# Kernel optimization log

Measured on AMD Instinct MI355X. Metric: run time of the kernel, lower is better.

## Reference

```python
import jax, jax.numpy as jnp
import numpy as np

N = 50000   # nodes
E = 800000  # edges
R = 8       # relations
B = 4       # bases
NEG = 0.2   # leaky relu slope


def setup_inputs() -> dict:
    key = jax.random.key(0)
    ks = jax.random.split(key, 20)
    s = 0.1
    rn = lambda k, sh: jax.random.normal(k, sh, dtype=jnp.float32) * s
    return {
        "x": jax.random.normal(ks[0], (N, 64), dtype=jnp.float32),
        "edge_index": jax.random.randint(ks[1], (2, E), 0, N),
        "edge_type": jax.random.randint(ks[2], (E,), 0, R),
        # RGCN layer 1 (64 -> 64), basis decomposition
        "basis1": rn(ks[3], (B, 64, 64)), "comp1": rn(ks[4], (R, B)),
        "root1": rn(ks[5], (64, 64)), "brg1": jnp.zeros((64,), jnp.float32),
        # GAT layer 1 (64 -> 32, heads=4, concat -> 128)
        "wg1": rn(ks[6], (64, 128)), "asrc1": rn(ks[7], (4, 32)),
        "adst1": rn(ks[8], (4, 32)), "bg1": jnp.zeros((128,), jnp.float32),
        # RGCN layer 2 (128 -> 32)
        "basis2": rn(ks[9], (B, 128, 32)), "comp2": rn(ks[10], (R, B)),
        "root2": rn(ks[11], (128, 32)), "brg2": jnp.zeros((32,), jnp.float32),
        # GAT layer 2 (32 -> 16, heads=4, concat=False -> mean)
        "wg2": rn(ks[12], (32, 64)), "asrc2": rn(ks[13], (4, 16)),
        "adst2": rn(ks[14], (4, 16)), "bg2": jnp.zeros((16,), jnp.float32),
    }


def rgcn(x, src, dst, etype, basis, comp, root, bias):
    """PyG RGCNConv with basis decomposition, aggr='mean' per relation."""
    n, f = x.shape
    weight = jnp.einsum('rb,bio->rio', comp, basis)          # [R, in, out]
    seg = dst * R + etype                                    # per (node, relation) segment
    msg = x[src]                                             # [E, in] gather
    sums = jax.ops.segment_sum(msg, seg, num_segments=n * R).reshape(n, R, f)
    cnt = jax.ops.segment_sum(jnp.ones((src.shape[0],), x.dtype), seg,
                              num_segments=n * R).reshape(n, R, 1)
    mean = sums / jnp.maximum(cnt, 1.0)                      # [N, R, in]
    return jnp.einsum('nri,rio->no', mean, weight) + x @ root + bias


def gat(x, src, dst, w, a_src, a_dst, bias, heads, out_ch, concat):
    """PyG GATConv: add self loops, edge softmax over incoming edges."""
    n = x.shape[0]
    loop = jnp.arange(n)
    s2 = jnp.concatenate([src, loop])
    d2 = jnp.concatenate([dst, loop])
    h = (x @ w).reshape(n, heads, out_ch)                    # [N, H, C]
    al_src = (h * a_src).sum(-1)                             # [N, H]
    al_dst = (h * a_dst).sum(-1)                             # [N, H]
    e = jax.nn.leaky_relu(al_src[s2] + al_dst[d2], NEG)      # [E2, H]
    m = jax.ops.segment_max(e, d2, num_segments=n)           # stable softmax per dst
    e = jnp.exp(e - m[d2])
    z = jax.ops.segment_sum(e, d2, num_segments=n)
    alpha = e / z[d2]                                        # [E2, H]
    msg = h[s2] * alpha[:, :, None]                          # [E2, H, C]
    out = jax.ops.segment_sum(msg, d2, num_segments=n)       # [N, H, C]
    out = out.reshape(n, heads * out_ch) if concat else out.mean(axis=1)
    return out + bias


def reference(x, edge_index, edge_type,
              basis1, comp1, root1, brg1, wg1, asrc1, adst1, bg1,
              basis2, comp2, root2, brg2, wg2, asrc2, adst2, bg2):
    src, dst = edge_index[0], edge_index[1]
    # i=0: RGCN + relu (dropout p=0)
    x = jax.nn.relu(rgcn(x, src, dst, edge_type, basis1, comp1, root1, brg1))
    # i=1 == 2*pairs-1: GAT concat, NO activation
    x = gat(x, src, dst, wg1, asrc1, adst1, bg1, heads=4, out_ch=32, concat=True)
    # i=2: RGCN + relu
    x = jax.nn.relu(rgcn(x, src, dst, edge_type, basis2, comp2, root2, brg2))
    # i=3: GAT mean-heads + relu
    x = jax.nn.relu(gat(x, src, dst, wg2, asrc2, adst2, bg2, heads=4, out_ch=16, concat=False))
    return jnp.tanh(x)
```

## Files before the change

kernel.cpp:

```cpp
#include <hip/hip_runtime.h>
#include <math.h>

#define NN 50000
#define EE 800000
#define RR 8
#define SLOPE 0.2f
#define SEGS (NN * RR)
#define NBLK ((SEGS + 255) / 256)
#define NTW ((NN + 63) / 64)

typedef __attribute__((ext_vector_type(8))) short bf16x8;
typedef __attribute__((ext_vector_type(4))) float f32x4;
typedef _Float16 f16;
typedef __attribute__((ext_vector_type(4))) _Float16 h4;
typedef __attribute__((ext_vector_type(8))) _Float16 h8;

__device__ __forceinline__ float leaky(float v) { return v >= 0.f ? v : SLOPE * v; }

__device__ __forceinline__ void fmacc(float4& a, const float4& v, float p) {
    a.x = fmaf(v.x, p, a.x);
    a.y = fmaf(v.y, p, a.y);
    a.z = fmaf(v.z, p, a.z);
    a.w = fmaf(v.w, p, a.w);
}

__device__ __forceinline__ void red4(float4& a, int m) {
    a.x += __shfl_xor(a.x, m);
    a.y += __shfl_xor(a.y, m);
    a.z += __shfl_xor(a.z, m);
    a.w += __shfl_xor(a.w, m);
}

__device__ __forceinline__ float4 h4tof4(h4 t) {
    return make_float4((float)t.x, (float)t.y, (float)t.z, (float)t.w);
}

__device__ __forceinline__ void split8(const float4& v0, const float4& v1,
                                       bf16x8& hi, bf16x8& lo) {
    float e[8] = {v0.x, v0.y, v0.z, v0.w, v1.x, v1.y, v1.z, v1.w};
    union { bf16x8 v; unsigned u[4]; } H, L;
#pragma unroll
    for (int j = 0; j < 4; j++) {
        unsigned b0 = __float_as_uint(e[2 * j]), b1 = __float_as_uint(e[2 * j + 1]);
        unsigned h0 = b0 & 0xFFFF0000u, h1 = b1 & 0xFFFF0000u;
        H.u[j] = (h0 >> 16) | h1;
        float l0 = e[2 * j] - __uint_as_float(h0);
        float l1 = e[2 * j + 1] - __uint_as_float(h1);
        L.u[j] = (__float_as_uint(l0) >> 16) | (__float_as_uint(l1) & 0xFFFF0000u);
    }
    hi = H.v;
    lo = L.v;
}

__global__ void k_count2(const int* __restrict__ dst, const int* __restrict__ et,
                         int* __restrict__ cnt2) {
    int e = blockIdx.x * 256 + threadIdx.x;
    if (e < EE) atomicAdd(&cnt2[dst[e] * RR + et[e]], 1);
}

__global__ void k_scanA(const int* __restrict__ cnt2, int* __restrict__ rp,
                        int* __restrict__ bsum) {
    __shared__ int sh[256];
    int t = threadIdx.x;
    int i = blockIdx.x * 256 + t;
    int v = (i < SEGS) ? cnt2[i] : 0;
    sh[t] = v;
    __syncthreads();
    for (int off = 1; off < 256; off <<= 1) {
        int u = (t >= off) ? sh[t - off] : 0;
        __syncthreads();
        sh[t] += u;
        __syncthreads();
    }
    if (i < SEGS) rp[i] = sh[t] - v;
    if (t == 255) bsum[blockIdx.x] = sh[255];
}

__global__ void k_scanB(int* __restrict__ bsum) {
    __shared__ int sh[256];
    int t = threadIdx.x;
    int loc[8];
    int s = 0;
#pragma unroll
    for (int i = 0; i < 8; i++) {
        int idx = t * 8 + i;
        int v = (idx < NBLK) ? bsum[idx] : 0;
        loc[i] = v;
        s += v;
    }
    sh[t] = s;
    __syncthreads();
    for (int off = 1; off < 256; off <<= 1) {
        int u = (t >= off) ? sh[t - off] : 0;
        __syncthreads();
        sh[t] += u;
        __syncthreads();
    }
    int run = sh[t] - s;
#pragma unroll
    for (int i = 0; i < 8; i++) {
        int idx = t * 8 + i;
        if (idx < NBLK) {
            int v = loc[i];
            bsum[idx] = run;
            run += v;
        }
    }
}

__global__ void k_scanC(int* __restrict__ rp, const int* __restrict__ bsum,
                        int* __restrict__ wo) {
    int i = blockIdx.x * 256 + threadIdx.x;
    if (i < SEGS) {
        int v = rp[i] + bsum[blockIdx.x];
        rp[i] = v;
        wo[i] = v;
    }
    if (i == 0) rp[SEGS] = EE;
}

__global__ void k_fill(const int* __restrict__ src, const int* __restrict__ dst,
                       const int* __restrict__ et, int* __restrict__ wo,
                       int* __restrict__ srcs2) {
    int e = blockIdx.x * 256 + threadIdx.x;
    if (e >= EE) return;
    int r = et[e];
    int seg = dst[e] * RR + r;
    int pos = atomicAdd(&wo[seg], 1);
    srcs2[pos] = (src[e] << 3) | r;
}

__global__ void k_prep(const float* __restrict__ wg1, const float* __restrict__ wg2,
                       const float* __restrict__ root1, const float* __restrict__ root2,
                       const float* __restrict__ basis1, const float* __restrict__ basis2,
                       const float* __restrict__ comp2,
                       const float* __restrict__ asrc1, const float* __restrict__ adst1,
                       const float* __restrict__ asrc2, const float* __restrict__ adst2,
                       float* __restrict__ Wcat2e, float* __restrict__ wg1r,
                       float* __restrict__ Wstk, float* __restrict__ U1p,
                       float* __restrict__ U2p, float* __restrict__ Wb1) {
    int idx = blockIdx.x * 256 + threadIdx.x;
    if (idx < 16384) {
        int h = idx >> 12, kc = idx & 4095;
        int k = kc >> 6, c = kc & 63;
        wg1r[idx] = (c < 32) ? wg1[k * 128 + h * 32 + c] : 0.f;
    } else if (idx < 24576) {
        int j = idx - 16384;
        int row = j >> 6, c = j & 63;
        int h = row >> 5, k = row & 31;
        Wstk[j] = (c < 16) ? wg2[k * 64 + h * 16 + c] : 0.f;
    } else if (idx < 32768) {
        int j = idx - 24576;
        int k = j >> 6, c = j & 63;
        Wcat2e[k * 320 + c] = (c < 32) ? root2[k * 32 + c] : 0.f;
    } else if (idx < 36864) {
        int j0 = idx - 32768;
        int k = j0 >> 6, j = j0 & 63;
        float s = 0.f;
        if (j < 8) {
            int h = j & 3;
            const float* a = (j < 4) ? asrc1 : adst1;
            for (int c = 0; c < 32; c++) s += wg1[k * 128 + h * 32 + c] * a[h * 32 + c];
        }
        U1p[j0] = s;
    } else if (idx < 38912) {
        int j0 = idx - 36864;
        int k = j0 >> 6, j = j0 & 63;
        float s = 0.f;
        if (j < 8) {
            int h = j & 3;
            const float* a = (j < 4) ? asrc2 : adst2;
            for (int c = 0; c < 16; c++) s += wg2[k * 64 + h * 16 + c] * a[h * 16 + c];
        }
        U2p[j0] = s;
    } else if (idx < 55296) {
        Wb1[idx - 38912] = basis1[idx - 38912];
    } else if (idx < 59392) {
        Wb1[idx - 38912] = root1[idx - 55296];
    } else if (idx < 92160) {
        int j = idx - 59392;
        int i = j >> 8, rc = j & 255;
        int r = rc >> 5, o = rc & 31;
        float acc = 0.f;
#pragma unroll
        for (int b = 0; b < 4; b++) acc += comp2[r * 4 + b] * basis2[b * 4096 + i * 32 + o];
        Wcat2e[i * 320 + 64 + rc] = acc;
    }
}

__global__ void k_pack(const float* __restrict__ Wb1, const float* __restrict__ wg1r,
                       const float* __restrict__ Wcat, short* __restrict__ pWb1,
                       short* __restrict__ pwg1r, short* __restrict__ pWcat) {
    int u = blockIdx.x * 256 + threadIdx.x;
    int lane = u & 63, pair = u >> 6;
    if (pair >= 136) return;
    int m = lane & 15, g = lane >> 4;
    const float* src;
    int ldB, col, k0;
    short* dst;
    if (pair < 40) {
        int ct = pair / 10, kc = pair % 10;
        src = Wb1; ldB = 64; col = ct * 16 + m; k0 = kc * 32 + g * 8;
        dst = pWb1 + pair * 1024 + lane * 8;
    } else if (pair < 56) {
        int q = pair - 40;
        int h = q >> 2, lp = q & 3, ct = lp >> 1, kc = lp & 1;
        src = wg1r + h * 4096; ldB = 64; col = ct * 16 + m; k0 = kc * 32 + g * 8;
        dst = pwg1r + q * 1024 + lane * 8;
    } else {
        int q = pair - 56;
        int p = q >> 4, lp = q & 15, ct = lp >> 2, kc = lp & 3;
        src = Wcat; ldB = 320; col = p * 64 + ct * 16 + m; k0 = kc * 32 + g * 8;
        dst = pWcat + q * 1024 + lane * 8;
    }
    float e[8];
#pragma unroll
    for (int r = 0; r < 8; r++) e[r] = src[(size_t)(k0 + r) * ldB + col];
    union { bf16x8 v; unsigned u4[4]; } H, L;
#pragma unroll
    for (int j = 0; j < 4; j++) {
        unsigned b0 = __float_as_uint(e[2 * j]), b1 = __float_as_uint(e[2 * j + 1]);
        unsigned h0 = b0 & 0xFFFF0000u, h1 = b1 & 0xFFFF0000u;
        H.u4[j] = (h0 >> 16) | h1;
        float l0 = e[2 * j] - __uint_as_float(h0);
        float l1 = e[2 * j + 1] - __uint_as_float(h1);
        L.u4[j] = (__float_as_uint(l0) >> 16) | (__float_as_uint(l1) & 0xFFFF0000u);
    }
    *(bf16x8*)dst = H.v;
    *(bf16x8*)(dst + 512) = L.v;
}

template <int KTOT, int NCOL, int ACT = 0, int OUTH = 0>
__global__ __launch_bounds__(256) void k_mfma(const float* __restrict__ X, int ldX, int xmb,
                                              const short* __restrict__ Bpk, int bmb,
                                              float* __restrict__ Y, int ldY, size_t ymb,
                                              const float* __restrict__ bias, int biasmb) {
    constexpr int NKC = KTOT / 32;
    constexpr int NCT = NCOL / 16;
    const int tid = threadIdx.x;
    const int wid = tid >> 6, lane = tid & 63;
    const int m = lane & 15, g = lane >> 4;
    const int mb = blockIdx.y;
    const int rowbase = blockIdx.x * 64 + wid * 16;
    if (rowbase >= NN) return;
    const float* Xm = X + (size_t)mb * xmb + (size_t)(rowbase + m) * ldX;
    const short* Bm = Bpk + (size_t)mb * bmb;

    f32x4 acc[NCT];
#pragma unroll
    for (int c = 0; c < NCT; c++) acc[c] = (f32x4){0.f, 0.f, 0.f, 0.f};

#pragma unroll
    for (int kc = 0; kc < NKC; kc++) {
        float4 v0 = *(const float4*)(Xm + kc * 32 + g * 8);
        float4 v1 = *(const float4*)(Xm + kc * 32 + g * 8 + 4);
        bf16x8 ah, al;
        split8(v0, v1, ah, al);
#pragma unroll
        for (int ct = 0; ct < NCT; ct++) {
            const short* bp = Bm + (size_t)(ct * NKC + kc) * 1024 + lane * 8;
            bf16x8 bh = *(const bf16x8*)bp;
            bf16x8 bl = *(const bf16x8*)(bp + 512);
            acc[ct] = __builtin_amdgcn_mfma_f32_16x16x32_bf16(ah, bh, acc[ct], 0, 0, 0);
            acc[ct] = __builtin_amdgcn_mfma_f32_16x16x32_bf16(al, bh, acc[ct], 0, 0, 0);
            acc[ct] = __builtin_amdgcn_mfma_f32_16x16x32_bf16(ah, bl, acc[ct], 0, 0, 0);
        }
    }

#pragma unroll
    for (int ct = 0; ct < NCT; ct++) {
        int col = ct * 16 + m;
        float bv = bias ? bias[mb * biasmb + col] : 0.f;
#pragma unroll
        for (int i = 0; i < 4; i++) {
            float o = acc[ct][i] + bv;
            if (ACT == 2) o = fmaxf(o, 0.f);
            if (OUTH) {
                f16* Yh = (f16*)Y;
                Yh[(size_t)mb * ymb + (size_t)(rowbase + g * 4 + i) * ldY + col] = (f16)o;
            } else {
                Y[(size_t)mb * ymb + (size_t)(rowbase + g * 4 + i) * ldY + col] = o;
            }
        }
    }
}

__global__ __launch_bounds__(256) void k_gagg1(const int* __restrict__ rp,
                                               const int* __restrict__ srcs2,
                                               const float* __restrict__ comp,
                                               const float* __restrict__ X,
                                               float* __restrict__ U) {
    __shared__ float4 sh_w[4][8];
    int wid = threadIdx.x >> 6, lane = threadIdx.x & 63;
    int n = blockIdx.x * 4 + wid;
    int rpv = (lane <= 8) ? rp[n * RR + lane] : 0;
    int nxt = __shfl(rpv, (lane + 1) & 63);
    if (lane < 8) {
        float inv = 1.f / (float)((nxt - rpv) > 0 ? (nxt - rpv) : 1);
        float4 c = *(const float4*)(comp + lane * 4);
        sh_w[wid][lane] = make_float4(c.x * inv, c.y * inv, c.z * inv, c.w * inv);
    }
    int q = lane & 15;
    int beg = rp[n * RR], end = rp[n * RR + RR];
    float4 a0 = make_float4(0.f, 0.f, 0.f, 0.f);
    float4 a1 = a0, a2 = a0, a3 = a0;
    int k = beg + (lane >> 4);
    for (; k + 4 < end; k += 8) {
        int key0 = srcs2[k], key1 = srcs2[k + 4];
        float4 w0 = sh_w[wid][key0 & 7], w1 = sh_w[wid][key1 & 7];
        float4 v0 = *(const float4*)(X + (size_t)(key0 >> 3) * 64 + q * 4);
        float4 v1 = *(const float4*)(X + (size_t)(key1 >> 3) * 64 + q * 4);
        fmacc(a0, v0, w0.x);
        fmacc(a1, v0, w0.y);
        fmacc(a2, v0, w0.z);
        fmacc(a3, v0, w0.w);
        fmacc(a0, v1, w1.x);
        fmacc(a1, v1, w1.y);
        fmacc(a2, v1, w1.z);
        fmacc(a3, v1, w1.w);
    }
    if (k < end) {
        int key0 = srcs2[k];
        float4 w0 = sh_w[wid][key0 & 7];
        float4 v0 = *(const float4*)(X + (size_t)(key0 >> 3) * 64 + q * 4);
        fmacc(a0, v0, w0.x);
        fmacc(a1, v0, w0.y);
        fmacc(a2, v0, w0.z);
        fmacc(a3, v0, w0.w);
    }
    red4(a0, 16); red4(a0, 32);
    red4(a1, 16); red4(a1, 32);
    red4(a2, 16); red4(a2, 32);
    red4(a3, 16); red4(a3, 32);
    if (lane < 16) {
        float* un = U + (size_t)n * 320;
        *(float4*)(un + 0 * 64 + q * 4) = a0;
        *(float4*)(un + 1 * 64 + q * 4) = a1;
        *(float4*)(un + 2 * 64 + q * 4) = a2;
        *(float4*)(un + 3 * 64 + q * 4) = a3;
        *(float4*)(un + 256 + q * 4) = *(const float4*)(X + (size_t)n * 64 + q * 4);
    }
}

__global__ __launch_bounds__(256) void k_alds1(const float* __restrict__ X,
                                               const float* __restrict__ U1p,
                                               float* __restrict__ alds,
                                               f16* __restrict__ x1h) {
    __shared__ float sUT[8 * 68];
    int tid = threadIdx.x;
    for (int i = tid; i < 512; i += 256) {
        int j = i >> 6, c = i & 63;
        sUT[j * 68 + c] = U1p[c * 64 + j];
    }
    __syncthreads();
    int lane = tid & 63, wid = tid >> 6;
    int n = blockIdx.x * 32 + wid * 8 + (lane >> 3);
    int q = lane & 7;
    float x[8];
    if (n < NN) {
        float4 v0 = *(const float4*)(X + (size_t)n * 64 + q * 8);
        float4 v1 = *(const float4*)(X + (size_t)n * 64 + q * 8 + 4);
        x[0] = v0.x; x[1] = v0.y; x[2] = v0.z; x[3] = v0.w;
        x[4] = v1.x; x[5] = v1.y; x[6] = v1.z; x[7] = v1.w;
        h8 hv;
#pragma unroll
        for (int c = 0; c < 8; c++) hv[c] = (f16)x[c];
        *(h8*)(x1h + (size_t)n * 64 + q * 8) = hv;
    } else {
#pragma unroll
        for (int c = 0; c < 8; c++) x[c] = 0.f;
    }
    float al[8];
#pragma unroll
    for (int j = 0; j < 8; j++) {
        const float* u = &sUT[j * 68 + q * 8];
        float s = 0.f;
#pragma unroll
        for (int c = 0; c < 8; c++) s += x[c] * u[c];
        al[j] = s;
    }
#pragma unroll
    for (int m = 1; m < 8; m <<= 1)
#pragma unroll
        for (int j = 0; j < 8; j++) al[j] += __shfl_xor(al[j], m);
    if (n < NN) alds[(size_t)n * 8 + q] = al[q];
}

__global__ __launch_bounds__(256) void k_final(const float* __restrict__ Xm,
                                               const float* __restrict__ Wstk,
                                               const float* __restrict__ bg2,
                                               float* __restrict__ out) {
    __shared__ float sWT[16 * 132];
    int tid = threadIdx.x;
    for (int i = tid; i < 2048; i += 256) {
        int c = i >> 7, k = i & 127;
        sWT[c * 132 + k] = Wstk[k * 64 + c];
    }
    __syncthreads();
    int lane = tid & 63, wid = tid >> 6;
    int n = blockIdx.x * 32 + wid * 8 + (lane >> 3);
    int q = lane & 7;
    float x[16];
    if (n < NN) {
#pragma unroll
        for (int t = 0; t < 4; t++) {
            float4 v = *(const float4*)(Xm + (size_t)n * 128 + t * 32 + q * 4);
            x[t * 4 + 0] = v.x; x[t * 4 + 1] = v.y; x[t * 4 + 2] = v.z; x[t * 4 + 3] = v.w;
        }
    } else {
#pragma unroll
        for (int k = 0; k < 16; k++) x[k] = 0.f;
    }
    float al[16];
#pragma unroll
    for (int c = 0; c < 16; c++) {
        float s = 0.f;
#pragma unroll
        for (int t = 0; t < 4; t++) {
            const float* w = &sWT[c * 132 + t * 32 + q * 4];
            s += x[t * 4 + 0] * w[0] + x[t * 4 + 1] * w[1] + x[t * 4 + 2] * w[2] +
                 x[t * 4 + 3] * w[3];
        }
        al[c] = s;
    }
#pragma unroll
    for (int m = 1; m < 8; m <<= 1)
#pragma unroll
        for (int c = 0; c < 16; c++) al[c] += __shfl_xor(al[c], m);
    if (n < NN && q < 4) {
        float4 bv = *(const float4*)(bg2 + q * 4);
        float4 v;
        v.x = tanhf(fmaxf(0.25f * al[q * 4 + 0] + bv.x, 0.f));
        v.y = tanhf(fmaxf(0.25f * al[q * 4 + 1] + bv.y, 0.f));
        v.z = tanhf(fmaxf(0.25f * al[q * 4 + 2] + bv.z, 0.f));
        v.w = tanhf(fmaxf(0.25f * al[q * 4 + 3] + bv.w, 0.f));
        *(float4*)(out + (size_t)n * 16 + q * 4) = v;
    }
}

__global__ __launch_bounds__(256) void k_agg2(const int* __restrict__ rp,
                                              const int* __restrict__ srcs2,
                                              const f16* __restrict__ y,
                                              const float* __restrict__ bias,
                                              const float* __restrict__ U2p,
                                              const float* __restrict__ x3prev,
                                              f16* __restrict__ x3h,
                                              float* __restrict__ alds) {
    __shared__ float sh_inv[4][8];
    int wid = threadIdx.x >> 6, lane = threadIdx.x & 63;
    int n = blockIdx.x * 4 + wid;
    int rpv = (lane <= 8) ? rp[n * RR + lane] : 0;
    int nxt = __shfl(rpv, (lane + 1) & 63);
    if (lane < 8) sh_inv[wid][lane] = 1.f / (float)((nxt - rpv) > 0 ? (nxt - rpv) : 1);
    int q = lane & 7;
    int beg = rp[n * RR], end = rp[n * RR + RR];
    float4 acc = make_float4(0.f, 0.f, 0.f, 0.f);
    int k = beg + (lane >> 3);
    for (; k + 8 < end; k += 16) {
        int key0 = srcs2[k], key1 = srcs2[k + 8];
        int s0 = key0 >> 3, s1 = key1 >> 3;
        int g0 = key0 & 7, g1 = key1 & 7;
        float e0 = sh_inv[wid][g0], e1 = sh_inv[wid][g1];
        float4 v0 = h4tof4(*(const h4*)(y + ((size_t)(g0 >> 1) * NN + s0) * 64 + (g0 & 1) * 32 + q * 4));
        float4 v1 = h4tof4(*(const h4*)(y + ((size_t)(g1 >> 1) * NN + s1) * 64 + (g1 & 1) * 32 + q * 4));
        fmacc(acc, v0, e0);
        fmacc(acc, v1, e1);
    }
    if (k < end) {
        int key0 = srcs2[k];
        int s0 = key0 >> 3;
        int g0 = key0 & 7;
        float4 v0 = h4tof4(*(const h4*)(y + ((size_t)(g0 >> 1) * NN + s0) * 64 + (g0 & 1) * 32 + q * 4));
        fmacc(acc, v0, sh_inv[wid][g0]);
    }
    red4(acc, 8);
    red4(acc, 16);
    red4(acc, 32);
    if (lane < 8) {
        float4 prev = *(const float4*)(x3prev + (size_t)n * 64 + q * 4);
        float4 b = *(const float4*)(bias + q * 4);
        float4 v;
        v.x = fmaxf(prev.x + acc.x + b.x, 0.f);
        v.y = fmaxf(prev.y + acc.y + b.y, 0.f);
        v.z = fmaxf(prev.z + acc.z + b.z, 0.f);
        v.w = fmaxf(prev.w + acc.w + b.w, 0.f);
        h4 hv = {(f16)v.x, (f16)v.y, (f16)v.z, (f16)v.w};
        *(h4*)(x3h + (size_t)n * 32 + q * 4) = hv;
        float al[8];
#pragma unroll
        for (int j = 0; j < 8; j++) {
            al[j] = fmaf(v.x, U2p[(q * 4 + 0) * 64 + j],
                    fmaf(v.y, U2p[(q * 4 + 1) * 64 + j],
                    fmaf(v.z, U2p[(q * 4 + 2) * 64 + j],
                         v.w * U2p[(q * 4 + 3) * 64 + j])));
        }
#pragma unroll
        for (int m = 1; m < 8; m <<= 1) {
#pragma unroll
            for (int j = 0; j < 8; j++) al[j] += __shfl_xor(al[j], m);
        }
        alds[n * 8 + q] = al[q];
    }
}

template <int F, int LDX = F>
__global__ __launch_bounds__(256) void k_gatx(const int* __restrict__ rp,
                                              const int* __restrict__ srcs2,
                                              const float* __restrict__ alds,
                                              const f16* __restrict__ X,
                                              float* __restrict__ msg) {
    constexpr int G = F / 4;
    constexpr int NG = 64 / G;
    int wid = threadIdx.x >> 6, lane = threadIdx.x & 63;
    int n = blockIdx.x * 4 + wid;
    if (n >= NN) return;
    int g = lane / G, q = lane % G;
    float4 ald4 = *(const float4*)(alds + n * 8 + 4);
    float4 acc0 = make_float4(0.f, 0.f, 0.f, 0.f);
    float4 acc1 = acc0, acc2 = acc0, acc3 = acc0;
    float4 z = make_float4(0.f, 0.f, 0.f, 0.f);
    if (g == 0) {
        float4 a4 = *(const float4*)(alds + n * 8);
        float4 xv = h4tof4(*(const h4*)(X + (size_t)n * LDX + q * 4));
        float p0 = __expf(leaky(a4.x + ald4.x));
        float p1 = __expf(leaky(a4.y + ald4.y));
        float p2 = __expf(leaky(a4.z + ald4.z));
        float p3 = __expf(leaky(a4.w + ald4.w));
        z = make_float4(p0, p1, p2, p3);
        fmacc(acc0, xv, p0);
        fmacc(acc1, xv, p1);
        fmacc(acc2, xv, p2);
        fmacc(acc3, xv, p3);
    }
    int beg = rp[n * RR], end = rp[n * RR + RR];
    int k = beg + g;
    for (; k + NG < end; k += 2 * NG) {
        int s0 = srcs2[k] >> 3, s1 = srcs2[k + NG] >> 3;
        float4 a0 = *(const float4*)(alds + s0 * 8);
        float4 a1 = *(const float4*)(alds + s1 * 8);
        float4 x0 = h4tof4(*(const h4*)(X + (size_t)s0 * LDX + q * 4));
        float4 x1v = h4tof4(*(const h4*)(X + (size_t)s1 * LDX + q * 4));
        float p00 = __expf(leaky(a0.x + ald4.x)), p01 = __expf(leaky(a0.y + ald4.y));
        float p02 = __expf(leaky(a0.z + ald4.z)), p03 = __expf(leaky(a0.w + ald4.w));
        float p10 = __expf(leaky(a1.x + ald4.x)), p11 = __expf(leaky(a1.y + ald4.y));
        float p12 = __expf(leaky(a1.z + ald4.z)), p13 = __expf(leaky(a1.w + ald4.w));
        z.x += p00 + p10;
        z.y += p01 + p11;
        z.z += p02 + p12;
        z.w += p03 + p13;
        fmacc(acc0, x0, p00);
        fmacc(acc1, x0, p01);
        fmacc(acc2, x0, p02);
        fmacc(acc3, x0, p03);
        fmacc(acc0, x1v, p10);
        fmacc(acc1, x1v, p11);
        fmacc(acc2, x1v, p12);
        fmacc(acc3, x1v, p13);
    }
    if (k < end) {
        int s0 = srcs2[k] >> 3;
        float4 a0 = *(const float4*)(alds + s0 * 8);
        float4 x0 = h4tof4(*(const h4*)(X + (size_t)s0 * LDX + q * 4));
        float p00 = __expf(leaky(a0.x + ald4.x)), p01 = __expf(leaky(a0.y + ald4.y));
        float p02 = __expf(leaky(a0.z + ald4.z)), p03 = __expf(leaky(a0.w + ald4.w));
        z.x += p00;
        z.y += p01;
        z.z += p02;
        z.w += p03;
        fmacc(acc0, x0, p00);
        fmacc(acc1, x0, p01);
        fmacc(acc2, x0, p02);
        fmacc(acc3, x0, p03);
    }
#pragma unroll
    for (int m = G; m < 64; m <<= 1) {
        red4(acc0, m);
        red4(acc1, m);
        red4(acc2, m);
        red4(acc3, m);
        red4(z, m);
    }
    if (g == 0) {
        float4 iz = make_float4(1.f / z.x, 1.f / z.y, 1.f / z.z, 1.f / z.w);
        float* mp = msg + (size_t)n * 4 * F + q * 4;
        *(float4*)(mp + 0 * F) = make_float4(acc0.x * iz.x, acc0.y * iz.x, acc0.z * iz.x, acc0.w * iz.x);
        *(float4*)(mp + 1 * F) = make_float4(acc1.x * iz.y, acc1.y * iz.y, acc1.z * iz.y, acc1.w * iz.y);
        *(float4*)(mp + 2 * F) = make_float4(acc2.x * iz.z, acc2.y * iz.z, acc2.z * iz.z, acc2.w * iz.z);
        *(float4*)(mp + 3 * F) = make_float4(acc3.x * iz.w, acc3.y * iz.w, acc3.z * iz.w, acc3.w * iz.w);
    }
}

extern "C" void kernel_launch(void* const* d_in, const int* in_sizes, int n_in,
                              void* d_out, int out_size, void* d_ws, size_t ws_size,
                              hipStream_t stream) {
    const float* x      = (const float*)d_in[0];
    const int*   ei     = (const int*)d_in[1];
    const int*   et     = (const int*)d_in[2];
    const float* basis1 = (const float*)d_in[3];
    const float* comp1  = (const float*)d_in[4];
    const float* root1  = (const float*)d_in[5];
    const float* brg1   = (const float*)d_in[6];
    const float* wg1    = (const float*)d_in[7];
    const float* asrc1  = (const float*)d_in[8];
    const float* adst1  = (const float*)d_in[9];
    const float* bg1    = (const float*)d_in[10];
    const float* basis2 = (const float*)d_in[11];
    const float* comp2  = (const float*)d_in[12];
    const float* root2  = (const float*)d_in[13];
    const float* brg2   = (const float*)d_in[14];
    const float* wg2    = (const float*)d_in[15];
    const float* asrc2  = (const float*)d_in[16];
    const float* adst2  = (const float*)d_in[17];
    const float* bg2    = (const float*)d_in[18];
    const int* src = ei;
    const int* dst = ei + EE;
    float* out = (float*)d_out;

    int* wsi = (int*)d_ws;
    size_t ioff = 0;
    auto ialloc = [&](size_t n) { int* p = wsi + ioff; ioff += (n + 3) & ~(size_t)3; return p; };
    int* cnt2 = ialloc(SEGS);
    int* rp   = ialloc(SEGS + 1);
    int* bsum = ialloc(2048);
    int* srcs2 = ialloc(EE);
    int* wo = cnt2;
    float* wsf = (float*)(wsi + ioff);
    size_t total_f = (ws_size - ioff * sizeof(int)) / sizeof(float);
    size_t P_f = (size_t)NN * 320;
    size_t need_f = P_f + (size_t)NN * 128
                  + 40960 + 20480 + 16384 + 8192 + 4096 + 2048
                  + (size_t)NN * 8
                  + 20480 + 8192 + 40960
                  + (size_t)NN * 32 + (size_t)NN * 16 + 64;
    if (total_f < need_f) return;
    size_t foff = 0;
    auto falloc = [&](size_t n) { float* p = wsf + foff; foff += (n + 3) & ~(size_t)3; return p; };
    float* P      = falloc(P_f);
    float* x2     = falloc((size_t)NN * 128);
    float* Wcat2e = falloc(40960);
    float* Wb1    = falloc(20480);
    float* wg1r   = falloc(16384);
    float* Wstk   = falloc(8192);
    float* U1p    = falloc(4096);
    float* U2p    = falloc(2048);
    float* alds   = falloc((size_t)NN * 8);
    short* Wb1pk  = (short*)falloc(20480);
    short* wg1rpk = (short*)falloc(8192);
    short* Wcatpk = (short*)falloc(40960);
    f16* x1h      = (f16*)falloc((size_t)NN * 32);
    f16* x3h      = (f16*)falloc((size_t)NN * 16);
    float* Ubuf = P;
    float* x1   = x2 + (size_t)NN * 64;
    float* msg1 = P;
    float* x3   = P;
    f16* ybuf3h = (f16*)(P + (size_t)NN * 64);
    float* msg2 = P + (size_t)NN * 64;

    const int EB = (EE + 255) / 256;
    const int NB4 = (NN + 3) / 4;
    const int NB32 = (NN + 31) / 32;

    hipMemsetAsync(cnt2, 0, SEGS * sizeof(int), stream);
    k_count2<<<EB, 256, 0, stream>>>(dst, et, cnt2);
    k_scanA<<<NBLK, 256, 0, stream>>>(cnt2, rp, bsum);
    k_scanB<<<1, 256, 0, stream>>>(bsum);
    k_scanC<<<NBLK, 256, 0, stream>>>(rp, bsum, wo);
    k_fill<<<EB, 256, 0, stream>>>(src, dst, et, wo, srcs2);
    k_prep<<<(92160 + 255) / 256, 256, 0, stream>>>(
        wg1, wg2, root1, root2, basis1, basis2, comp2, asrc1, adst1, asrc2, adst2,
        Wcat2e, wg1r, Wstk, U1p, U2p, Wb1);
    k_pack<<<34, 256, 0, stream>>>(Wb1, wg1r, Wcat2e, Wb1pk, wg1rpk, Wcatpk);

    k_gagg1<<<NB4, 256, 0, stream>>>(rp, srcs2, comp1, x, Ubuf);
    k_mfma<320, 64, 2><<<dim3(NTW, 1), 256, 0, stream>>>(Ubuf, 320, 0, Wb1pk, 0,
                                                         x1, 64, 0, brg1, 0);

    k_alds1<<<NB32, 256, 0, stream>>>(x1, U1p, alds, x1h);
    k_gatx<64, 64><<<NB4, 256, 0, stream>>>(rp, srcs2, alds, x1h, msg1);
    k_mfma<64, 32, 0><<<dim3(NTW, 4), 256, 0, stream>>>(msg1, 256, 64, wg1rpk, 4096,
                                                        x2, 128, 32, bg1, 32);

    k_mfma<128, 64, 0, 0><<<dim3(NTW, 1), 256, 0, stream>>>(x2, 128, 0, Wcatpk, 0,
                                                            P, 64, 0, nullptr, 0);
    k_mfma<128, 64, 0, 1><<<dim3(NTW, 4), 256, 0, stream>>>(x2, 128, 0, Wcatpk + 16384, 16384,
                                                            (float*)ybuf3h, 64, (size_t)NN * 64,
                                                            nullptr, 0);
    k_agg2<<<NB4, 256, 0, stream>>>(rp, srcs2, ybuf3h, brg2, U2p, x3, x3h, alds);

    k_gatx<32, 32><<<NB4, 256, 0, stream>>>(rp, srcs2, alds, x3h, msg2);
    k_final<<<NB32, 256, 0, stream>>>(msg2, Wstk, bg2, out);
}
```

Before: 459.4 us.

## Replace global-atomic CSR fill with two-pass bucketed scatter using LDS atomics

The per-edge global atomicAdd scatter into CSR segments is replaced by two passes. The first partitions edges into 98 coarse destination buckets (512 nodes each) using LDS histograms and one global atomic per bucket per block. The second sorts each bucket into its segments with LDS atomics. This cuts global atomic contention and random writes, but adds an extra pass over a new record buffer and leaves only 98 blocks for the second pass.

New measurement: 441.2 us. 4.0% less time.

```diff
diff --git a/kernel.cpp b/kernel.cpp
--- a/kernel.cpp
+++ b/kernel.cpp
@@ -8,6 +8,9 @@
 #define SEGS (NN * RR)
 #define NBLK ((SEGS + 255) / 256)
 #define NTW ((NN + 63) / 64)
+#define NBUK 98
+#define SEGB 4096
+#define EB4 ((EE + 4095) / 4096)
 
 typedef __attribute__((ext_vector_type(8))) short bf16x8;
 typedef __attribute__((ext_vector_type(4))) float f32x4;
@@ -108,26 +111,78 @@
     }
 }
 
-__global__ void k_scanC(int* __restrict__ rp, const int* __restrict__ bsum,
-                        int* __restrict__ wo) {
+__global__ void k_scanC(int* __restrict__ rp, const int* __restrict__ bsum) {
     int i = blockIdx.x * 256 + threadIdx.x;
-    if (i < SEGS) {
-        int v = rp[i] + bsum[blockIdx.x];
-        rp[i] = v;
-        wo[i] = v;
-    }
+    if (i < SEGS) rp[i] += bsum[blockIdx.x];
     if (i == 0) rp[SEGS] = EE;
 }
 
-__global__ void k_fill(const int* __restrict__ src, const int* __restrict__ dst,
-                       const int* __restrict__ et, int* __restrict__ wo,
-                       int* __restrict__ srcs2) {
-    int e = blockIdx.x * 256 + threadIdx.x;
-    if (e >= EE) return;
-    int r = et[e];
-    int seg = dst[e] * RR + r;
-    int pos = atomicAdd(&wo[seg], 1);
-    srcs2[pos] = (src[e] << 3) | r;
+__global__ void k_initcb(const int* __restrict__ rp, int* __restrict__ cbcur) {
+    int t = threadIdx.x;
+    if (t < NBUK) cbcur[t] = rp[t * SEGB];
+}
+
+__global__ __launch_bounds__(256) void k_fillA(const int* __restrict__ src,
+                                               const int* __restrict__ dst,
+                                               const int* __restrict__ et,
+                                               int* __restrict__ cbcur,
+                                               int* __restrict__ recbuf) {
+    __shared__ int hist[NBUK], lcur[NBUK], gres[NBUK];
+    int tid = threadIdx.x;
+    int e0 = blockIdx.x * 4096;
+    int cnt = EE - e0;
+    if (cnt > 4096) cnt = 4096;
+    for (int i = tid; i < NBUK; i += 256) { hist[i] = 0; lcur[i] = 0; }
+    __syncthreads();
+    int myb[16], myrec[16];
+#pragma unroll
+    for (int j = 0; j < 16; j++) {
+        int i = tid + j * 256;
+        if (i < cnt) {
+            int e = e0 + i;
+            int d = dst[e];
+            int b = d >> 9;
+            myb[j] = b;
+            myrec[j] = ((d & 511) << 19) | (src[e] << 3) | et[e];
+            atomicAdd(&hist[b], 1);
+        } else {
+            myb[j] = -1;
+            myrec[j] = 0;
+        }
+    }
+    __syncthreads();
+    if (tid < NBUK) gres[tid] = atomicAdd(&cbcur[tid], hist[tid]);
+    __syncthreads();
+#pragma unroll
+    for (int j = 0; j < 16; j++) {
+        if (myb[j] >= 0) {
+            int p = atomicAdd(&lcur[myb[j]], 1);
+            recbuf[gres[myb[j]] + p] = myrec[j];
+        }
+    }
+}
+
+__global__ __launch_bounds__(256) void k_fillB(const int* __restrict__ rp,
+                                               const int* __restrict__ recbuf,
+                                               int* __restrict__ srcs2) {
+    __shared__ int cur[SEGB];
+    int b = blockIdx.x;
+    int segbase = b * SEGB;
+    int nseg = SEGS - segbase;
+    if (nseg > SEGB) nseg = SEGB;
+    int base = rp[segbase];
+    int tid = threadIdx.x;
+    for (int s = tid; s < SEGB; s += 256)
+        cur[s] = (s < nseg) ? (rp[segbase + s] - base) : 0;
+    __syncthreads();
+    int limit = rp[segbase + nseg];
+    int cnt = limit - base;
+    for (int i = tid; i < cnt; i += 256) {
+        int rec = recbuf[base + i];
+        int segl = ((rec >> 19) << 3) | (rec & 7);
+        int p = atomicAdd(&cur[segl], 1);
+        srcs2[base + p] = rec & 0x7FFFF;
+    }
 }
 
 __global__ void k_prep(const float* __restrict__ wg1, const float* __restrict__ wg2,
@@ -623,7 +678,8 @@
     int* rp   = ialloc(SEGS + 1);
     int* bsum = ialloc(2048);
     int* srcs2 = ialloc(EE);
-    int* wo = cnt2;
+    int* recbuf = ialloc(EE);
+    int* cbcur = ialloc(128);
     float* wsf = (float*)(wsi + ioff);
     size_t total_f = (ws_size - ioff * sizeof(int)) / sizeof(float);
     size_t P_f = (size_t)NN * 320;
@@ -664,8 +720,10 @@
     k_count2<<<EB, 256, 0, stream>>>(dst, et, cnt2);
     k_scanA<<<NBLK, 256, 0, stream>>>(cnt2, rp, bsum);
     k_scanB<<<1, 256, 0, stream>>>(bsum);
-    k_scanC<<<NBLK, 256, 0, stream>>>(rp, bsum, wo);
-    k_fill<<<EB, 256, 0, stream>>>(src, dst, et, wo, srcs2);
+    k_scanC<<<NBLK, 256, 0, stream>>>(rp, bsum);
+    k_initcb<<<1, 128, 0, stream>>>(rp, cbcur);
+    k_fillA<<<EB4, 256, 0, stream>>>(src, dst, et, cbcur, recbuf);
+    k_fillB<<<NBUK, 256, 0, stream>>>(rp, recbuf, srcs2);
     k_prep<<<(92160 + 255) / 256, 256, 0, stream>>>(
         wg1, wg2, root1, root2, basis1, basis2, comp2, asrc1, adst1, asrc2, adst2,
         Wcat2e, wg1r, Wstk, U1p, U2p, Wb1);
```
